# Kernel tuning notes

Measured on AMD Instinct MI355X. Metric: run time of the kernel, lower is better.

Reference implementation:

```python
import jax, jax.numpy as jnp
import numpy as np

K = 20      # kNN neighbors
H = 4       # attention heads
EPS = 1e-5  # BatchNorm eps
NEG = 0.2   # LeakyReLU negative slope


def lrelu(x):
    return jnp.where(x >= 0, x, NEG * x)


def bn(x, g, b):
    # eval-mode BatchNorm: running_mean=0, running_var=1
    return x * (g / jnp.sqrt(1.0 + EPS)) + b


def knn_idx(x):
    # x: (B, N, C) -> (B, N, K) indices of K nearest neighbors (incl. self)
    inner = -2.0 * jnp.einsum('bnc,bmc->bnm', x, x)
    xx = jnp.sum(x * x, axis=-1)
    pd = -xx[:, :, None] - inner - xx[:, None, :]  # negative squared distance
    return jax.lax.top_k(pd, K)[1]


def edge_conv(x, w, g, b):
    # EdgeConv: gather kNN features, cat(nbr-ctr, ctr), 1x1 conv, BN, LeakyReLU, max over K
    idx = knn_idx(x)                                   # (B,N,K)
    nbr = jax.vmap(lambda f, i: f[i])(x, idx)          # (B,N,K,C)
    ctr = jnp.broadcast_to(x[:, :, None, :], nbr.shape)
    e = jnp.concatenate([nbr - ctr, ctr], axis=-1)     # (B,N,K,2C)
    h = lrelu(bn(jnp.einsum('bnkc,oc->bnko', e, w), g, b))
    return jnp.max(h, axis=2)                          # (B,N,Cout)


def mha(x, w_in, b_in, w_out, b_out):
    # Faithful to source: (B,N,E) fed to nn.MultiheadAttention with batch_first=False,
    # so seq length L=B and batch=N (attention mixes across the batch axis).
    L, Nb, E = x.shape
    d = E // H
    qkv = x @ w_in.T + b_in
    q, k, v = jnp.split(qkv, 3, axis=-1)
    q = q.reshape(L, Nb, H, d) * (1.0 / np.sqrt(d))
    k = k.reshape(L, Nb, H, d)
    v = v.reshape(L, Nb, H, d)
    a = jax.nn.softmax(jnp.einsum('lnhd,mnhd->nhlm', q, k), axis=-1)
    o = jnp.einsum('nhlm,mnhd->lnhd', a, v).reshape(L, Nb, E)
    return o @ w_out.T + b_out


def setup_inputs():
    ks = iter(jax.random.split(jax.random.key(0), 64))
    def rn(shape, s=0.05):
        return jax.random.normal(next(ks), shape, jnp.float32) * s
    def gamma(c):
        return 1.0 + rn((c,), 0.1)
    B, N = 8, 1024
    inp = {'x': rn((B, N, 3), 1.0)}
    for i, (ci, co) in enumerate([(6, 64), (128, 64), (128, 128), (256, 256)], 1):
        inp[f'w{i}'] = rn((co, ci)); inp[f'g{i}'] = gamma(co); inp[f'b{i}'] = rn((co,))
    for i, e in enumerate([64, 64, 128, 256], 1):
        inp[f'a{i}_wi'] = rn((3 * e, e)); inp[f'a{i}_bi'] = rn((3 * e,))
        inp[f'a{i}_wo'] = rn((e, e));     inp[f'a{i}_bo'] = rn((e,))
    inp['w5'] = rn((1024, 512)); inp['g5'] = gamma(1024); inp['b5'] = rn((1024,))
    inp['l1w'] = rn((512, 2048)); inp['g6'] = gamma(512); inp['b6'] = rn((512,))
    inp['l2w'] = rn((256, 512)); inp['l2b'] = rn((256,))
    inp['g7'] = gamma(256); inp['b7'] = rn((256,))
    inp['l3w'] = rn((40, 256)); inp['l3b'] = rn((40,))
    return inp


def reference(x, w1, g1, b1, a1_wi, a1_bi, a1_wo, a1_bo,
              w2, g2, b2, a2_wi, a2_bi, a2_wo, a2_bo,
              w3, g3, b3, a3_wi, a3_bi, a3_wo, a3_bo,
              w4, g4, b4, a4_wi, a4_bi, a4_wo, a4_bo,
              w5, g5, b5, l1w, g6, b6, l2w, l2b, g7, b7, l3w, l3b):
    x1 = edge_conv(x, w1, g1, b1)
    x1 = mha(x1, a1_wi, a1_bi, a1_wo, a1_bo) + x1
    x2 = edge_conv(x1, w2, g2, b2)
    x2 = mha(x2, a2_wi, a2_bi, a2_wo, a2_bo) + x2
    x3 = edge_conv(x2, w3, g3, b3)
    x3 = mha(x3, a3_wi, a3_bi, a3_wo, a3_bo) + x3
    x4 = edge_conv(x3, w4, g4, b4)
    x4 = mha(x4, a4_wi, a4_bi, a4_wo, a4_bo) + x4
    h = lrelu(bn(jnp.concatenate([x1, x2, x3, x4], axis=-1) @ w5.T, g5, b5))  # (B,N,1024)
    feat = jnp.concatenate([jnp.max(h, axis=1), jnp.mean(h, axis=1)], axis=-1)  # (B,2048)
    h = lrelu(bn(feat @ l1w.T, g6, b6))
    h = lrelu(bn(h @ l2w.T + l2b, g7, b7))  # dropout is eval-mode identity
    return h @ l3w.T + l3b  # (B, 40)
```

## Files before the change

### kernel.cpp

```cpp
#include <hip/hip_runtime.h>
#include <hip/hip_bf16.h>

#define B_ 8
#define N_ 1024
#define K_ 20
#define BN_ (B_*N_)

#define BN_SCALE 0.9999950000374997f

typedef __attribute__((ext_vector_type(8))) short short8;
typedef __attribute__((ext_vector_type(4))) float f32x4;

__device__ __forceinline__ float US2F(unsigned short u) {
    union { unsigned u; float f; } c; c.u = ((unsigned)u) << 16; return c.f;
}
__device__ __forceinline__ unsigned short F2BF(float f) {
    union { float f; unsigned u; } c; c.f = f;
    unsigned r = c.u + 0x7FFF + ((c.u >> 16) & 1);
    return (unsigned short)(r >> 16);
}

__device__ __forceinline__ void ldsld16(const unsigned short* g, unsigned short* l) {
    __builtin_amdgcn_global_load_lds(
        (const __attribute__((address_space(1))) void*)g,
        (__attribute__((address_space(3))) void*)l, 16, 0, 0);
}

struct DetP { const unsigned short* g[7]; };
__device__ __forceinline__ int det_isbf(const DetP& dp) {
    int cnt = 0;
    #pragma unroll
    for (int i = 0; i < 7; i++) {
        float v = US2F(dp.g[i][0]);
        if (v > 0.5f && v < 1.5f) cnt++;
    }
    return cnt >= 4;
}

struct TPar { const void* src; void* dst; int O, I, blk0, mode; };
struct TList { TPar p[44]; };
struct TrP { const void* src; float* dst; int O, I, bx, blk0; };

__global__ __launch_bounds__(256) void k_prep(TList tl, int nent,
                                              TrP q0, TrP q1, TrP q2,
                                              int nbp, int nbtr,
                                              const void* x0, DetP dp,
                                              unsigned short* __restrict__ xa,
                                              unsigned short* __restrict__ xb,
                                              float* __restrict__ xx1) {
    __shared__ int sbf;
    if (threadIdx.x == 0) sbf = det_isbf(dp);
    __syncthreads();
    const int isbf = sbf;
    auto ld0 = [&](int idx) {
        return isbf ? US2F(((const unsigned short*)x0)[idx])
                    : ((const float*)x0)[idx];
    };
    const int bid = blockIdx.x;
    if (bid >= nbp + nbtr) {
        int blk = bid - nbp - nbtr;
        if (blk >= (BN_ * 32) / 256) {
            int i = (blk - (BN_ * 32) / 256) * 256 + threadIdx.x;
            if (i >= BN_) return;
            float s = 0.f;
            #pragma unroll
            for (int c = 0; c < 3; c++) { float v = ld0(i * 3 + c); s += v * v; }
            xx1[i] = s;
            return;
        }
        const int e = blk * 256 + threadIdx.x;
        const int i = e >> 5, p = e & 31;
        unsigned short va = 0, vb = 0;
        if (p < 9) {
            const int seg = p / 3, c = p - seg * 3;
            const float v = ld0(i * 3 + c);
            const unsigned short h = F2BF(v);
            const unsigned short l = F2BF(v - US2F(h));
            va = (seg == 1) ? l : h;
            vb = (seg < 2) ? h : l;
        }
        xa[e] = va; xb[e] = vb;
        return;
    }
    if (bid >= nbp) {
        int blk = bid - nbp;
        TrP p = q0;
        if (blk >= q2.blk0) p = q2; else if (blk >= q1.blk0) p = q1;
        blk -= p.blk0;
        const int tx = threadIdx.x & 31, ty = threadIdx.x >> 5;
        const int bi = blk % p.bx, bo = blk / p.bx;
        const int i0 = bi * 32, o0 = bo * 32;
        __shared__ float s[32][33];
        #pragma unroll
        for (int r = 0; r < 4; r++) {
            const int o = o0 + ty + r * 8, i = i0 + tx;
            if (o < p.O && i < p.I) {
                const size_t e = (size_t)o * p.I + i;
                s[ty + r * 8][tx] = isbf ? US2F(((const unsigned short*)p.src)[e])
                                         : ((const float*)p.src)[e];
            }
        }
        __syncthreads();
        #pragma unroll
        for (int r = 0; r < 4; r++) {
            const int i = i0 + ty + r * 8, o = o0 + tx;
            if (i < p.I && o < p.O) p.dst[(size_t)i * p.O + o] = s[tx][ty + r * 8];
        }
        return;
    }
    int blk = bid;
    int wi = 0;
    for (int j = nent - 1; j >= 0; j--) { if (blk >= tl.p[j].blk0) { wi = j; break; } }
    const TPar p = tl.p[wi];
    int e = (blk - p.blk0) * 256 + threadIdx.x;
    int n = p.O * p.I;
    if (e >= n) return;
    if (p.mode == 4) { ((float*)p.dst)[e] = 0.f; return; }
    int o = e / p.I, i = e - o * p.I;
    float v = isbf ? US2F(((const unsigned short*)p.src)[e])
                   : ((const float*)p.src)[e];
    if (p.mode == 0) {
        ((float*)p.dst)[(size_t)i * p.O + o] = v;
    } else if (p.mode == 2) {
        ((unsigned short*)p.dst)[e] = F2BF(v);
    } else {
        const int C = p.I >> 1;
        if (i < C) ((unsigned short*)p.dst)[(size_t)o * C + i] = F2BF(v);
        else       ((unsigned short*)p.dst)[(size_t)(p.O + o) * C + (i - C)] = F2BF(v);
    }
}

template<int KP, int TM, int TN>
__device__ __forceinline__ void pdm_dev(int bid,
                                        const unsigned short* __restrict__ xa,
                                        const unsigned short* __restrict__ xb,
                                        const float* __restrict__ xx,
                                        float* __restrict__ pd) {
    const int b = bid & 7;
    const int tt = bid >> 3;
    const int rb = (tt >> 3) * TM, cb = (tt & 7) * TN;
    const unsigned short* Ab = xa + (size_t)b * N_ * KP;
    const unsigned short* Bb = xb + (size_t)b * N_ * KP;
    const float* xxb = xx + (size_t)b * N_;
    const int t = threadIdx.x;
    __shared__ __align__(16) unsigned short As[2][TM * 32];
    __shared__ __align__(16) unsigned short Bs[2][TN * 32];
    const int w = t >> 6, lane = t & 63;
    constexpr int QR = TM / 2, QC = TN / 2;
    constexpr int MR = QR / 16, NR = QC / 16;
    const int wr = (w & 1) * QR, wc = (w >> 1) * QC;
    const int fr = lane & 15, q = lane >> 4;
    f32x4 acc[MR][NR] = {};

    auto STAGE = [&](int buf, int k0) {
        constexpr int AT = TM * 4;
        #pragma unroll
        for (int R = 0; R < (AT + 255) / 256; R++) {
            const int G = t + R * 256;
            if (AT >= (R + 1) * 256 || G < AT) {
                const int m = G >> 2, gs = (G & 3) ^ ((m >> 1) & 3);
                ldsld16(&Ab[(size_t)(rb + m) * KP + k0 + gs * 8], &As[buf][w * 512 + R * 2048]);
            }
        }
        constexpr int BT = TN * 4;
        #pragma unroll
        for (int R = 0; R < (BT + 255) / 256; R++) {
            const int G = t + R * 256;
            if (BT >= (R + 1) * 256 || G < BT) {
                const int n = G >> 2, gs = (G & 3) ^ ((n >> 1) & 3);
                ldsld16(&Bb[(size_t)(cb + n) * KP + k0 + gs * 8], &Bs[buf][w * 512 + R * 2048]);
            }
        }
    };

    constexpr int NT = KP / 32;
    STAGE(0, 0);
    asm volatile("s_waitcnt vmcnt(0)" ::: "memory");
    __builtin_amdgcn_s_barrier();
    int cur = 0;
    for (int ts = 0; ts < NT; ++ts) {
        if (ts + 1 < NT) STAGE(cur ^ 1, (ts + 1) * 32);
        short8 af[MR], bfr[NR];
        #pragma unroll
        for (int mi = 0; mi < MR; mi++) {
            const int r = wr + mi * 16 + fr;
            af[mi] = *reinterpret_cast<const short8*>(&As[cur][r * 32 + ((q ^ ((r >> 1) & 3)) << 3)]);
        }
        #pragma unroll
        for (int ni = 0; ni < NR; ni++) {
            const int r = wc + ni * 16 + fr;
            bfr[ni] = *reinterpret_cast<const short8*>(&Bs[cur][r * 32 + ((q ^ ((r >> 1) & 3)) << 3)]);
        }
        #pragma unroll
        for (int mi = 0; mi < MR; mi++) {
            #pragma unroll
            for (int ni = 0; ni < NR; ni++)
                acc[mi][ni] = __builtin_amdgcn_mfma_f32_16x16x32_bf16(af[mi], bfr[ni], acc[mi][ni], 0, 0, 0);
        }
        asm volatile("s_waitcnt vmcnt(0)" ::: "memory");
        __builtin_amdgcn_s_barrier();
        cur ^= 1;
    }
    float* pdb = pd + (size_t)b * N_ * N_;
    const int cr = (lane >> 4) * 4, cc = lane & 15;
    #pragma unroll
    for (int mi = 0; mi < MR; mi++) {
        #pragma unroll
        for (int ni = 0; ni < NR; ni++) {
            #pragma unroll
            for (int r = 0; r < 4; r++) {
                const int row = rb + wr + mi * 16 + cr + r;
                const int col = cb + wc + ni * 16 + cc;
                pdb[(size_t)row * N_ + col] = 2.f * acc[mi][ni][r] - xxb[col];
            }
        }
    }
}

template<int KD, int NC, int TM, int TN, bool CATA, bool POOL, int SPLIT>
__device__ __forceinline__ void gemm_dev(int bx, int by,
                                         const unsigned short* __restrict__ A,
                                         const unsigned short* __restrict__ A2,
                                         const unsigned short* __restrict__ A3,
                                         const unsigned short* __restrict__ A4,
                                         const unsigned short* __restrict__ Bw,
                                         const float* __restrict__ bias,
                                         const float* __restrict__ resid,
                                         float* __restrict__ Cout,
                                         float* __restrict__ Cz, int yco,
                                         int scale_cols, float qs,
                                         const float* __restrict__ gamma,
                                         const float* __restrict__ beta,
                                         unsigned short* __restrict__ obf,
                                         unsigned* __restrict__ pmaxu,
                                         float* __restrict__ psum,
                                         unsigned short* __restrict__ sxa,
                                         unsigned short* __restrict__ sxb,
                                         float* __restrict__ xxo) {
    const int t = threadIdx.x;
    const int rb = bx * TM, cb = by * TN;
    const int w = t >> 6, lane = t & 63;
    constexpr int QR = TM / 2, QC = TN / 2;
    constexpr int MR = QR / 16, NR = QC / 16;
    const int wr = (w & 1) * QR, wc = (w >> 1) * QC;
    const int fr = lane & 15, q = lane >> 4, fq = q * 8;
    f32x4 acc[MR][NR] = {};
    if constexpr (KD % 32 == 0) {
        __shared__ __align__(16) unsigned short As[2][TM * 32];
        __shared__ __align__(16) unsigned short Bs[2][TN * 32];
        auto STAGE = [&](int buf, int k0) {
            const unsigned short* Asrc = A; int AC = KD, ac0 = k0;
            if constexpr (CATA) {
                if (k0 >= 256)      { Asrc = A4; AC = 256; ac0 = k0 - 256; }
                else if (k0 >= 128) { Asrc = A3; AC = 128; ac0 = k0 - 128; }
                else if (k0 >= 64)  { Asrc = A2; AC = 64;  ac0 = k0 - 64; }
                else                { Asrc = A;  AC = 64;  ac0 = k0; }
            }
            constexpr int AT = TM * 4;
            #pragma unroll
            for (int R = 0; R < (AT + 255) / 256; R++) {
                const int G = t + R * 256;
                if (AT >= (R + 1) * 256 || G < AT) {
                    const int m = G >> 2, gs = (G & 3) ^ ((m >> 1) & 3);
                    ldsld16(&Asrc[(size_t)(rb + m) * AC + ac0 + gs * 8], &As[buf][w * 512 + R * 2048]);
                }
            }
            constexpr int BT = TN * 4;
            #pragma unroll
            for (int R = 0; R < (BT + 255) / 256; R++) {
                const int G = t + R * 256;
                if (BT >= (R + 1) * 256 || G < BT) {
                    const int n = G >> 2, gs = (G & 3) ^ ((n >> 1) & 3);
                    ldsld16(&Bw[(size_t)(cb + n) * KD + k0 + gs * 8], &Bs[buf][w * 512 + R * 2048]);
                }
            }
        };
        constexpr int NT = KD / 32;
        STAGE(0, 0);
        asm volatile("s_waitcnt vmcnt(0)" ::: "memory");
        __builtin_amdgcn_s_barrier();
        int cur = 0;
        for (int ts = 0; ts < NT; ++ts) {
            if (ts + 1 < NT) STAGE(cur ^ 1, (ts + 1) * 32);
            short8 af[MR], bfr[NR];
            #pragma unroll
            for (int mi = 0; mi < MR; mi++) {
                const int r = wr + mi * 16 + fr;
                af[mi] = *reinterpret_cast<const short8*>(&As[cur][r * 32 + ((q ^ ((r >> 1) & 3)) << 3)]);
            }
            #pragma unroll
            for (int ni = 0; ni < NR; ni++) {
                const int r = wc + ni * 16 + fr;
                bfr[ni] = *reinterpret_cast<const short8*>(&Bs[cur][r * 32 + ((q ^ ((r >> 1) & 3)) << 3)]);
            }
            #pragma unroll
            for (int mi = 0; mi < MR; mi++) {
                #pragma unroll
                for (int ni = 0; ni < NR; ni++)
                    acc[mi][ni] = __builtin_amdgcn_mfma_f32_16x16x32_bf16(af[mi], bfr[ni], acc[mi][ni], 0, 0, 0);
            }
            asm volatile("s_waitcnt vmcnt(0)" ::: "memory");
            __builtin_amdgcn_s_barrier();
            cur ^= 1;
        }
    } else {
        __shared__ __align__(16) unsigned short As[TM * 40];
        __shared__ __align__(16) unsigned short Bs[TN * 40];
        for (int k0 = 0; k0 < KD; k0 += 32) {
            __syncthreads();
            #pragma unroll
            for (int u = t; u < TM * 4; u += 256) {
                const int m = u >> 2, c = (u & 3) * 8;
                #pragma unroll
                for (int j = 0; j < 8; j++) {
                    const int kk = k0 + c + j;
                    As[m * 40 + c + j] = (kk < KD) ? A[(size_t)(rb + m) * KD + kk] : (unsigned short)0;
                }
            }
            #pragma unroll
            for (int u = t; u < TN * 4; u += 256) {
                const int n = u >> 2, c = (u & 3) * 8;
                const int gn = cb + n;
                if (gn < NC) {
                    #pragma unroll
                    for (int j = 0; j < 8; j++) {
                        const int kk = k0 + c + j;
                        Bs[n * 40 + c + j] = (kk < KD) ? Bw[(size_t)gn * KD + kk] : (unsigned short)0;
                    }
                } else {
                    short8 z = {};
                    *reinterpret_cast<short8*>(&Bs[n * 40 + c]) = z;
                }
            }
            __syncthreads();
            short8 af[MR], bfr[NR];
            #pragma unroll
            for (int mi = 0; mi < MR; mi++)
                af[mi] = *reinterpret_cast<const short8*>(&As[(wr + mi * 16 + fr) * 40 + fq]);
            #pragma unroll
            for (int ni = 0; ni < NR; ni++)
                bfr[ni] = *reinterpret_cast<const short8*>(&Bs[(wc + ni * 16 + fr) * 40 + fq]);
            #pragma unroll
            for (int mi = 0; mi < MR; mi++) {
                #pragma unroll
                for (int ni = 0; ni < NR; ni++)
                    acc[mi][ni] = __builtin_amdgcn_mfma_f32_16x16x32_bf16(af[mi], bfr[ni], acc[mi][ni], 0, 0, 0);
            }
        }
    }
    const int cr = (lane >> 4) * 4, cc = lane & 15;
    if constexpr (POOL) {
        const int bidx = rb >> 10;
        #pragma unroll
        for (int ni = 0; ni < NR; ni++) {
            const int col = cb + wc + ni * 16 + cc;
            const float gm = gamma[col] * BN_SCALE, bt = beta[col];
            float sm = 0.f, mxv = -3e38f;
            #pragma unroll
            for (int mi = 0; mi < MR; mi++) {
                #pragma unroll
                for (int r = 0; r < 4; r++) {
                    float v = acc[mi][ni][r] * gm + bt;
                    v = v >= 0.f ? v : 0.2f * v;
                    sm += v; mxv = fmaxf(mxv, v);
                }
            }
            sm += __shfl_xor(sm, 16, 64);
            sm += __shfl_xor(sm, 32, 64);
            mxv = fmaxf(mxv, __shfl_xor(mxv, 16, 64));
            mxv = fmaxf(mxv, __shfl_xor(mxv, 32, 64));
            if (lane < 16) {
                atomicAdd(&psum[bidx * 1024 + col], sm);
                unsigned tb = __float_as_uint(mxv);
                tb = (tb & 0x80000000u) ? ~tb : (tb | 0x80000000u);
                atomicMax(&pmaxu[bidx * 1024 + col], tb);
            }
        }
    } else {
        float sx[MR][4] = {};
        #pragma unroll
        for (int mi = 0; mi < MR; mi++) {
            #pragma unroll
            for (int ni = 0; ni < NR; ni++) {
                #pragma unroll
                for (int r = 0; r < 4; r++) {
                    const int row = rb + wr + mi * 16 + cr + r;
                    const int col = cb + wc + ni * 16 + cc;
                    if (col < NC) {
                        float v = acc[mi][ni][r] + (bias ? bias[col] : 0.f);
                        if (col < scale_cols) v *= qs;
                        if (resid) v += resid[(size_t)row * NC + col];
                        if (gamma) {
                            v = v * (gamma[col] * BN_SCALE) + beta[col];
                            v = v >= 0.f ? v : 0.2f * v;
                        }
                        if (yco > 0) {
                            if (col < yco) Cout[(size_t)row * yco + col] = v;
                            else           Cz[(size_t)row * yco + (col - yco)] = v;
                        } else {
                            Cout[(size_t)row * NC + col] = v;
                        }
                        if (obf) obf[(size_t)row * NC + col] = F2BF(v);
                        if constexpr (SPLIT > 0) {
                            constexpr int KP2 = 3 * SPLIT;
                            const unsigned short h = F2BF(v);
                            const unsigned short l = F2BF(v - US2F(h));
                            sxa[(size_t)row * KP2 + 0 * SPLIT + col] = h;
                            sxa[(size_t)row * KP2 + 1 * SPLIT + col] = l;
                            sxa[(size_t)row * KP2 + 2 * SPLIT + col] = h;
                            sxb[(size_t)row * KP2 + 0 * SPLIT + col] = h;
                            sxb[(size_t)row * KP2 + 1 * SPLIT + col] = h;
                            sxb[(size_t)row * KP2 + 2 * SPLIT + col] = l;
                            sx[mi][r] += v * v;
                        }
                    }
                }
            }
        }
        if constexpr (SPLIT > 0) {
            #pragma unroll
            for (int mi = 0; mi < MR; mi++) {
                #pragma unroll
                for (int r = 0; r < 4; r++) {
                    float s = sx[mi][r];
                    s += __shfl_xor(s, 1, 64);
                    s += __shfl_xor(s, 2, 64);
                    s += __shfl_xor(s, 4, 64);
                    s += __shfl_xor(s, 8, 64);
                    if ((lane & 15) == 0)
                        atomicAdd(&xxo[rb + wr + mi * 16 + cr + r], s);
                }
            }
        }
    }
}

template<int KD, int NC, int TM, int TN, bool CATA = false, bool POOL = false, int SPLIT = 0, bool AFF = false>
__global__ __launch_bounds__(256) void k_gemmb(const unsigned short* __restrict__ A,
                                               const unsigned short* __restrict__ A2,
                                               const unsigned short* __restrict__ A3,
                                               const unsigned short* __restrict__ A4,
                                               const unsigned short* __restrict__ Bw,
                                               const float* __restrict__ bias,
                                               const float* __restrict__ resid,
                                               float* __restrict__ Cout,
                                               int scale_cols, float qs,
                                               const float* __restrict__ gamma,
                                               const float* __restrict__ beta,
                                               unsigned short* __restrict__ obf,
                                               unsigned* __restrict__ pmaxu,
                                               float* __restrict__ psum,
                                               unsigned short* __restrict__ sxa,
                                               unsigned short* __restrict__ sxb,
                                               float* __restrict__ xxo) {
    int bx = blockIdx.x;
    if constexpr (AFF) bx = (bx & 7) * (gridDim.x >> 3) + (bx >> 3);
    gemm_dev<KD, NC, TM, TN, CATA, POOL, SPLIT>(bx, blockIdx.y,
        A, A2, A3, A4, Bw, bias, resid, Cout, nullptr, 0, scale_cols, qs, gamma, beta,
        obf, pmaxu, psum, sxa, sxb, xxo);
}

template<int KP, int KDY, int NCY, int TMY, int TNY>
__global__ __launch_bounds__(256) void k_pdmyz(const unsigned short* __restrict__ xa,
                                               const unsigned short* __restrict__ xb,
                                               const float* __restrict__ xx,
                                               float* __restrict__ pd,
                                               const unsigned short* __restrict__ Ay,
                                               const unsigned short* __restrict__ Bwy,
                                               float* __restrict__ Cy,
                                               float* __restrict__ Cz, int yco, int gxy) {
    if ((int)blockIdx.x < 512) { pdm_dev<KP, 128, 128>(blockIdx.x, xa, xb, xx, pd); return; }
    const int g = blockIdx.x - 512;
    const int batch = g & 7, rem = g >> 3;
    const int rpb = gxy >> 3;
    const int bx = batch * rpb + rem % rpb;
    const int by = rem / rpb;
    gemm_dev<KDY, NCY, TMY, TNY, false, false, 0>(bx, by,
        Ay, nullptr, nullptr, nullptr, Bwy, nullptr, nullptr, Cy, Cz, yco, 0, 1.f,
        nullptr, nullptr, nullptr, nullptr, nullptr, nullptr, nullptr, nullptr);
}

template<int CO>
__global__ __launch_bounds__(256) void k_seledge(const float* __restrict__ pd,
                                                 const float* __restrict__ y,
                                                 const float* __restrict__ z,
                                                 const float* __restrict__ g,
                                                 const float* __restrict__ bb,
                                                 float* __restrict__ out,
                                                 unsigned short* __restrict__ outb) {
    const int t = threadIdx.x;
    const int w = t >> 6, lane = t & 63;
    const int blk = blockIdx.x;
    const int b = blk & 7;
    const int i0 = (b << 10) + ((blk >> 3) << 2);
    const int bbase = b << 10;
    __shared__ int sidx[4][K_];
    {
        const int i = i0 + w;
        const float* row = pd + (size_t)b * N_ * N_ + (size_t)(i & 1023) * N_;
        unsigned key[16];
        #pragma unroll
        for (int q = 0; q < 16; q++) {
            const int j = q * 64 + lane;
            unsigned bits = __float_as_uint(row[j]);
            bits = (bits & 0x80000000u) ? ~bits : (bits | 0x80000000u);
            key[q] = (bits & 0xFFFFFC00u) | (unsigned)(N_ - 1 - j);
        }
        int myj = 0;
        for (int kk = 0; kk < K_; kk++) {
            unsigned m = key[0];
            #pragma unroll
            for (int u = 1; u < 16; u++) m = key[u] > m ? key[u] : m;
            #pragma unroll
            for (int s = 1; s < 64; s <<= 1) {
                unsigned o = (unsigned)__shfl_xor((int)m, s, 64);
                m = o > m ? o : m;
            }
            const int j = N_ - 1 - (int)(m & 1023u);
            if (lane == kk) myj = j;
            #pragma unroll
            for (int u = 0; u < 16; u++)
                if (key[u] == m) key[u] = 0u;
        }
        if (lane < K_) sidx[w][lane] = myj;
    }
    __syncthreads();
    constexpr int TPP = CO / 4;
    if (t < 4 * TPP) {
        const int p = t / TPP;
        const int cw = (t % TPP) * 4;
        const int ig = i0 + p;
        float4 m = {-3e38f, -3e38f, -3e38f, -3e38f};
        #pragma unroll 4
        for (int k = 0; k < K_; k++) {
            const int jg = bbase + sidx[p][k];
            const float4 yv = *reinterpret_cast<const float4*>(&y[(size_t)jg * CO + cw]);
            m.x = fmaxf(m.x, yv.x); m.y = fmaxf(m.y, yv.y);
            m.z = fmaxf(m.z, yv.z); m.w = fmaxf(m.w, yv.w);
        }
        const float4 yi = *reinterpret_cast<const float4*>(&y[(size_t)ig * CO + cw]);
        const float4 zi = *reinterpret_cast<const float4*>(&z[(size_t)ig * CO + cw]);
        const float4 gv = *reinterpret_cast<const float4*>(&g[cw]);
        const float4 bv = *reinterpret_cast<const float4*>(&bb[cw]);
        float vals[4] = {m.x - yi.x + zi.x, m.y - yi.y + zi.y,
                         m.z - yi.z + zi.z, m.w - yi.w + zi.w};
        float gs[4] = {gv.x, gv.y, gv.z, gv.w};
        float bs[4] = {bv.x, bv.y, bv.z, bv.w};
        float4 o;
        float* op = &o.x;
        #pragma unroll
        for (int j = 0; j < 4; j++) {
            float h = vals[j] * (gs[j] * BN_SCALE) + bs[j];
            op[j] = h >= 0.f ? h : 0.2f * h;
        }
        *reinterpret_cast<float4*>(&out[(size_t)ig * CO + cw]) = o;
        #pragma unroll
        for (int j = 0; j < 4; j++) outb[(size_t)ig * CO + cw + j] = F2BF(op[j]);
    }
}

template<int E>
__global__ __launch_bounds__(256) void k_attn(const float* __restrict__ qkv,
                                              unsigned short* __restrict__ o) {
    constexpr int H = 4, D = E / H, L = 8;
    const int n = blockIdx.x;
    const int t = threadIdx.x;
    const int h = t >> 6, lane = t & 63;
    __shared__ float sq[L][3 * E];
    __shared__ float so[L][E];
    for (int u = t; u < L * 3 * E; u += 256) {
        int l = u / (3 * E), r = u - l * (3 * E);
        sq[l][r] = qkv[(size_t)(l * N_ + n) * (3 * E) + r];
    }
    __syncthreads();
    const int l = lane >> 3, m = lane & 7;
    float s = 0.f;
    #pragma unroll 8
    for (int dd = 0; dd < D; dd++)
        s += sq[l][h * D + dd] * sq[m][E + h * D + dd];
    float mx = s;
    #pragma unroll
    for (int st = 1; st < 8; st <<= 1) mx = fmaxf(mx, __shfl_xor(mx, st, 64));
    float e = expf(s - mx);
    float sum = e;
    #pragma unroll
    for (int st = 1; st < 8; st <<= 1) sum += __shfl_xor(sum, st, 64);
    const float p = e / sum;
    float pm[8];
    #pragma unroll
    for (int mm = 0; mm < 8; mm++) pm[mm] = __shfl(p, (lane & 56) | mm, 64);
    #pragma unroll
    for (int j = 0; j < D / 8; j++) {
        const int dd = m + 8 * j;
        float a = 0.f;
        #pragma unroll
        for (int mm = 0; mm < 8; mm++) a += pm[mm] * sq[mm][2 * E + h * D + dd];
        so[l][h * D + dd] = a;
    }
    __syncthreads();
    for (int u = t; u < L * E; u += 256) {
        int l2 = u / E, e2 = u - l2 * E;
        o[(size_t)(l2 * N_ + n) * E + e2] = F2BF(so[l2][e2]);
    }
}

template<int E, int SPLIT>
__global__ __launch_bounds__(256) void k_attnout(const float* __restrict__ qkv,
                                                 const unsigned short* __restrict__ wo,
                                                 const float* __restrict__ bo,
                                                 float* __restrict__ x,
                                                 unsigned short* __restrict__ xob,
                                                 unsigned short* __restrict__ sxa,
                                                 unsigned short* __restrict__ sxb,
                                                 float* __restrict__ xxo) {
    constexpr int H = 4, D = E / H, L = 8;
    const int n = blockIdx.x;
    const int t = threadIdx.x;
    const int h = t >> 6, lane = t & 63;
    __shared__ float sq[L][3 * E];
    __shared__ float so[L][E];
    __shared__ unsigned short swo[E][E + 8];
    __shared__ float sxx[L];
    for (int u = t; u < L * 3 * E; u += 256) {
        int l = u / (3 * E), r = u - l * (3 * E);
        sq[l][r] = qkv[(size_t)(l * N_ + n) * (3 * E) + r];
    }
    for (int u = t; u < E * E; u += 256) swo[u / E][u % E] = wo[u];
    if (t < L) sxx[t] = 0.f;
    __syncthreads();
    const int l = lane >> 3, m = lane & 7;
    float s = 0.f;
    #pragma unroll 8
    for (int dd = 0; dd < D; dd++)
        s += sq[l][h * D + dd] * sq[m][E + h * D + dd];
    float mx = s;
    #pragma unroll
    for (int st = 1; st < 8; st <<= 1) mx = fmaxf(mx, __shfl_xor(mx, st, 64));
    float e = expf(s - mx);
    float sum = e;
    #pragma unroll
    for (int st = 1; st < 8; st <<= 1) sum += __shfl_xor(sum, st, 64);
    const float p = e / sum;
    float pm[8];
    #pragma unroll
    for (int mm = 0; mm < 8; mm++) pm[mm] = __shfl(p, (lane & 56) | mm, 64);
    #pragma unroll
    for (int j = 0; j < D / 8; j++) {
        const int dd = m + 8 * j;
        float a = 0.f;
        #pragma unroll
        for (int mm = 0; mm < 8; mm++) a += pm[mm] * sq[mm][2 * E + h * D + dd];
        so[l][h * D + dd] = a;
    }
    __syncthreads();
    for (int u = t; u < L * E; u += 256)
        so[u / E][u % E] = US2F(F2BF(so[u / E][u % E]));
    __syncthreads();
    constexpr int PT = (L * E) / 256;
    #pragma unroll
    for (int it = 0; it < PT; it++) {
        const int item = t + it * 256;
        const int ll = item / E, ee = item % E;
        float acc = 0.f;
        #pragma unroll 16
        for (int c = 0; c < E; c++)
            acc += so[ll][c] * US2F(swo[ee][c]);
        const int row = ll * N_ + n;
        const float v = acc + bo[ee] + x[(size_t)row * E + ee];
        x[(size_t)row * E + ee] = v;
        xob[(size_t)row * E + ee] = F2BF(v);
        if constexpr (SPLIT > 0) {
            constexpr int KP2 = 3 * SPLIT;
            const unsigned short hh = F2BF(v);
            const unsigned short lo = F2BF(v - US2F(hh));
            sxa[(size_t)row * KP2 + 0 * SPLIT + ee] = hh;
            sxa[(size_t)row * KP2 + 1 * SPLIT + ee] = lo;
            sxa[(size_t)row * KP2 + 2 * SPLIT + ee] = hh;
            sxb[(size_t)row * KP2 + 0 * SPLIT + ee] = hh;
            sxb[(size_t)row * KP2 + 1 * SPLIT + ee] = hh;
            sxb[(size_t)row * KP2 + 2 * SPLIT + ee] = lo;
            float vs = v * v;
            #pragma unroll
            for (int st = 1; st < 64; st <<= 1) vs += __shfl_xor(vs, st, 64);
            if (lane == 0) atomicAdd(&sxx[ll], vs);
        }
    }
    if constexpr (SPLIT > 0) {
        __syncthreads();
        if (t < L) xxo[t * N_ + n] = sxx[t];
    }
}

__global__ __launch_bounds__(256) void k_fc1(const unsigned* __restrict__ pmaxu,
                                             const float* __restrict__ psum,
                                             const float* __restrict__ l1wT,
                                             const float* __restrict__ g6, const float* __restrict__ b6,
                                             float* __restrict__ f1) {
    int oc = blockIdx.x, b = blockIdx.y, t = threadIdx.x;
    __shared__ float fin[2048];
    __shared__ float ps[4][64];
    for (int u = t; u < 2048; u += 256) {
        float v;
        if (u < 1024) {
            unsigned tb = pmaxu[b * 1024 + u];
            unsigned bits = (tb & 0x80000000u) ? (tb & 0x7FFFFFFFu) : ~tb;
            v = __uint_as_float(bits);
        } else {
            v = psum[b * 1024 + (u - 1024)] * (1.f / 1024.f);
        }
        fin[u] = v;
    }
    __syncthreads();
    int ol = t & 63, kc = t >> 6;
    int o = oc * 64 + ol;
    float acc = 0.f;
    for (int c = kc * 512; c < kc * 512 + 512; c++) acc += fin[c] * l1wT[(size_t)c * 512 + o];
    ps[kc][ol] = acc;
    __syncthreads();
    if (t < 64) {
        int oo = oc * 64 + t;
        float a = ps[0][t] + ps[1][t] + ps[2][t] + ps[3][t];
        float h = a * (g6[oo] * BN_SCALE) + b6[oo];
        f1[b * 512 + oo] = h >= 0.f ? h : 0.2f * h;
    }
}

__global__ __launch_bounds__(256) void k_fc23(const float* __restrict__ f1, const float* __restrict__ l2wT,
                                              const float* __restrict__ l2b,
                                              const float* __restrict__ g7, const float* __restrict__ b7,
                                              const float* __restrict__ l3wT, const float* __restrict__ l3b,
                                              void* __restrict__ out, DetP dp) {
    int b = blockIdx.x, t = threadIdx.x;
    __shared__ float fin[512];
    __shared__ float f2s[256];
    __shared__ int sbf;
    if (t == 0) sbf = det_isbf(dp);
    for (int u = t; u < 512; u += 256) fin[u] = f1[b * 512 + u];
    __syncthreads();
    {
        float acc = 0.f;
        for (int c = 0; c < 512; c++) acc += fin[c] * l2wT[(size_t)c * 256 + t];
        acc += l2b[t];
        float h = acc * (g7[t] * BN_SCALE) + b7[t];
        f2s[t] = h >= 0.f ? h : 0.2f * h;
    }
    __syncthreads();
    if (t < 40) {
        float acc = 0.f;
        for (int c = 0; c < 256; c++) acc += f2s[c] * l3wT[(size_t)c * 40 + t];
        acc += l3b[t];
        if (sbf) ((__hip_bfloat16*)out)[b * 40 + t] = __float2bfloat16(acc);
        else     ((float*)out)[b * 40 + t] = acc;
    }
}

extern "C" void kernel_launch(void* const* d_in, const int* in_sizes, int n_in,
                              void* d_out, int out_size, void* d_ws, size_t ws_size,
                              hipStream_t stream) {
    auto us = [&](int i) { return (const unsigned short*)d_in[i]; };

    float* ws = (float*)d_ws;
    size_t off = 0;
    auto A = [&](size_t n) { float* p = ws + off; off += (n + 3) & ~(size_t)3; return p; };
    auto AU = [&](size_t n) { return (unsigned short*)A((n + 1) / 2); };
    float* x1   = A((size_t)BN_ * 64);
    float* x2   = A((size_t)BN_ * 64);
    float* x3   = A((size_t)BN_ * 128);
    float* x4   = A((size_t)BN_ * 256);
    float* pd   = A((size_t)BN_ * 1024);
    float* f1   = A(8 * 512);
    float* xx   = A(4 * BN_);
    float* qkvw = A((size_t)BN_ * 768);
    unsigned short* xa = AU((size_t)BN_ * 384);
    unsigned short* xb = AU((size_t)BN_ * 384);
    unsigned short* xf0b = AU((size_t)BN_ * 3);
    unsigned short* x1b  = AU((size_t)BN_ * 64);
    unsigned short* x2b  = AU((size_t)BN_ * 64);
    unsigned short* x3b  = AU((size_t)BN_ * 128);
    unsigned short* x4b  = AU((size_t)BN_ * 256);
    unsigned short* owb  = AU((size_t)BN_ * 256);
    unsigned* pmaxu = (unsigned*)A(8 * 1024);
    float*    psum  = A(8 * 1024);
    unsigned short* w1yzb = AU(128 * 3);
    unsigned short* w2yzb = AU(128 * 64);
    unsigned short* w3yzb = AU(256 * 64);
    unsigned short* w4yzb = AU(512 * 128);
    unsigned short* a1wib = AU(192 * 64);  unsigned short* a1wob = AU(64 * 64);
    unsigned short* a2wib = AU(192 * 64);  unsigned short* a2wob = AU(64 * 64);
    unsigned short* a3wib = AU(384 * 128); unsigned short* a3wob = AU(128 * 128);
    unsigned short* a4wib = AU(768 * 256); unsigned short* a4wob = AU(256 * 256);
    unsigned short* w5b   = AU(1024 * 512);
    float* l1wT  = A(2048 * 512);
    float* l2wT  = A(512 * 256);
    float* l3wT  = A(256 * 40);
    float* g1f = A(64);   float* b1f = A(64);
    float* g2f = A(64);   float* b2f = A(64);
    float* g3f = A(128);  float* b3f = A(128);
    float* g4f = A(256);  float* b4f = A(256);
    float* bi1 = A(192);  float* bo1 = A(64);
    float* bi2 = A(192);  float* bo2 = A(64);
    float* bi3 = A(384);  float* bo3 = A(128);
    float* bi4 = A(768);  float* bo4 = A(256);
    float* g5f = A(1024); float* b5f = A(1024);
    float* g6f = A(512);  float* b6f = A(512);
    float* l2bf = A(256);
    float* g7f = A(256);  float* b7f = A(256);
    float* l3bf = A(40);

    float* xx1 = xx;              float* xx2 = xx + BN_;
    float* xx3 = xx + 2 * BN_;    float* xx4 = xx + 3 * BN_;

    float* yy = qkvw;
    float* zz = qkvw + (size_t)BN_ * 256;

    DetP dp{{us(2), us(5), us(8), us(11), us(30), us(33), us(37)}};

    TList tl; int nb = 0; int k = 0;
    auto add = [&](int i, void* dst, int O, int I, int mode) {
        tl.p[k].src = d_in[i]; tl.p[k].dst = dst; tl.p[k].O = O; tl.p[k].I = I;
        tl.p[k].blk0 = nb; tl.p[k].mode = mode;
        nb += (O * I + 255) / 256; k++;
    };
    add(0,  xf0b,  BN_ * 3, 1, 2);
    add(0,  pmaxu, 16384, 1, 4);
    add(1,  w1yzb, 64, 6, 3);
    add(4,  w2yzb, 64, 128, 3);
    add(7,  w3yzb, 128, 128, 3);
    add(10, w4yzb, 256, 256, 3);
    add(13, a1wib, 192, 64, 2);
    add(15, a1wob, 64, 64, 2);
    add(17, a2wib, 192, 64, 2);
    add(19, a2wob, 64, 64, 2);
    add(21, a3wib, 384, 128, 2);
    add(23, a3wob, 128, 128, 2);
    add(25, a4wib, 768, 256, 2);
    add(27, a4wob, 256, 256, 2);
    add(29, w5b,   1024, 512, 2);
    add(2,  g1f, 64, 1, 0);   add(3,  b1f, 64, 1, 0);
    add(5,  g2f, 64, 1, 0);   add(6,  b2f, 64, 1, 0);
    add(8,  g3f, 128, 1, 0);  add(9,  b3f, 128, 1, 0);
    add(11, g4f, 256, 1, 0);  add(12, b4f, 256, 1, 0);
    add(14, bi1, 192, 1, 0);  add(16, bo1, 64, 1, 0);
    add(18, bi2, 192, 1, 0);  add(20, bo2, 64, 1, 0);
    add(22, bi3, 384, 1, 0);  add(24, bo3, 128, 1, 0);
    add(26, bi4, 768, 1, 0);  add(28, bo4, 256, 1, 0);
    add(30, g5f, 1024, 1, 0); add(31, b5f, 1024, 1, 0);
    add(33, g6f, 512, 1, 0);  add(34, b6f, 512, 1, 0);
    add(36, l2bf, 256, 1, 0);
    add(37, g7f, 256, 1, 0);  add(38, b7f, 256, 1, 0);
    add(40, l3bf, 40, 1, 0);

    TrP tp1{d_in[32], l1wT, 512, 2048, 2048 / 32, 0};
    TrP tp2{d_in[35], l2wT, 256, 512,  512 / 32,  (2048 / 32) * (512 / 32)};
    TrP tp3{d_in[39], l3wT, 40,  256,  256 / 32,  tp2.blk0 + (512 / 32) * (256 / 32)};
    const int trblocks = tp3.blk0 + (256 / 32) * ((40 + 31) / 32);
    const int splblocks = (BN_ * 32) / 256 + 32;
    k_prep<<<nb + trblocks + splblocks, 256, 0, stream>>>(
        tl, k, tp1, tp2, tp3, nb, trblocks, d_in[0], dp, xa, xb, xx1);

    const unsigned short* N0 = nullptr;
    unsigned short* U0 = nullptr;
    unsigned* NU = nullptr; float* NF = nullptr;

    k_pdmyz<32, 3, 128, 64, 64><<<512 + 256, 256, 0, stream>>>(xa, xb, xx1, pd, xf0b, w1yzb, yy, zz, 64, 128);
    k_seledge<64><<<2048, 256, 0, stream>>>(pd, yy, zz, g1f, b1f, x1, x1b);
    k_gemmb<64, 192, 64, 64, false, false, 0, true><<<dim3(128, 3), 256, 0, stream>>>(x1b, N0, N0, N0, a1wib, bi1, nullptr, qkvw, 64, 0.25f, nullptr, nullptr, nullptr, NU, NF, U0, U0, NF);
    k_attnout<64, 64><<<N_, 256, 0, stream>>>(qkvw, a1wob, bo1, x1, x1b, xa, xb, xx2);

    k_pdmyz<192, 64, 128, 64, 64><<<512 + 256, 256, 0, stream>>>(xa, xb, xx2, pd, x1b, w2yzb, yy, zz, 64, 128);
    k_seledge<64><<<2048, 256, 0, stream>>>(pd, yy, zz, g2f, b2f, x2, x2b);
    k_gemmb<64, 192, 64, 64, false, false, 0, true><<<dim3(128, 3), 256, 0, stream>>>(x2b, N0, N0, N0, a2wib, bi2, nullptr, qkvw, 64, 0.25f, nullptr, nullptr, nullptr, NU, NF, U0, U0, NF);
    k_attnout<64, 64><<<N_, 256, 0, stream>>>(qkvw, a2wob, bo2, x2, x2b, xa, xb, xx3);

    k_pdmyz<192, 64, 256, 64, 64><<<512 + 512, 256, 0, stream>>>(xa, xb, xx3, pd, x2b, w3yzb, yy, zz, 128, 128);
    k_seledge<128><<<2048, 256, 0, stream>>>(pd, yy, zz, g3f, b3f, x3, x3b);
    k_gemmb<128, 384, 64, 128, false, false, 0, true><<<dim3(128, 3), 256, 0, stream>>>(x3b, N0, N0, N0, a3wib, bi3, nullptr, qkvw, 128, 0.17677669529663687f, nullptr, nullptr, nullptr, NU, NF, U0, U0, NF);
    k_attnout<128, 128><<<N_, 256, 0, stream>>>(qkvw, a3wob, bo3, x3, x3b, xa, xb, xx4);

    k_pdmyz<384, 128, 512, 128, 128><<<512 + 256, 256, 0, stream>>>(xa, xb, xx4, pd, x3b, w4yzb, yy, zz, 256, 64);
    k_seledge<256><<<2048, 256, 0, stream>>>(pd, yy, zz, g4f, b4f, x4, x4b);
    k_gemmb<256, 768, 64, 128, false, false, 0, true><<<dim3(128, 6), 256, 0, stream>>>(x4b, N0, N0, N0, a4wib, bi4, nullptr, qkvw, 256, 0.125f, nullptr, nullptr, nullptr, NU, NF, U0, U0, NF);
    k_attn<256><<<N_, 256, 0, stream>>>(qkvw, owb);
    k_gemmb<256, 256, 64, 128, false, false, 0, true><<<dim3(128, 2), 256, 0, stream>>>(owb, N0, N0, N0, a4wob, bo4, x4, x4, 0, 1.f, nullptr, nullptr, x4b, NU, NF, U0, U0, NF);

    k_gemmb<512, 1024, 128, 128, true, true, 0, true><<<dim3(64, 8), 256, 0, stream>>>(
        x1b, x2b, x3b, x4b, w5b, nullptr, nullptr, nullptr, 0, 1.f, g5f, b5f, nullptr, pmaxu, psum, U0, U0, NF);
    k_fc1<<<dim3(8, 8), 256, 0, stream>>>(pmaxu, psum, l1wT, g6f, b6f, f1);
    k_fc23<<<8, 256, 0, stream>>>(f1, l2wT, l2bf, g7f, b7f, l3wT, l3bf, d_out, dp);
}
```

Before: 476.0 us.

## Spread weight preparation across later kernels as auxiliary blocks

Weight conversion and transpose work that used to run entirely in the first prep kernel is split into three groups. The weights needed later (layer 2-3 conv/attention, fc1 transpose, layer-4 attention and w5) are now handled by extra blocks appended to the first pairwise-distance and selection kernels. This shortens the serial prep launch and overlaps that work with kernels that may leave CUs idle. In exchange those kernels get extra parameters, and each auxiliary block reruns the dtype detection.

```diff
diff --git a/kernel.cpp b/kernel.cpp
--- a/kernel.cpp
+++ b/kernel.cpp
@@ -38,77 +38,10 @@
 }
 
 struct TPar { const void* src; void* dst; int O, I, blk0, mode; };
-struct TList { TPar p[44]; };
+struct TList { TPar p[32]; };
 struct TrP { const void* src; float* dst; int O, I, bx, blk0; };
 
-__global__ __launch_bounds__(256) void k_prep(TList tl, int nent,
-                                              TrP q0, TrP q1, TrP q2,
-                                              int nbp, int nbtr,
-                                              const void* x0, DetP dp,
-                                              unsigned short* __restrict__ xa,
-                                              unsigned short* __restrict__ xb,
-                                              float* __restrict__ xx1) {
-    __shared__ int sbf;
-    if (threadIdx.x == 0) sbf = det_isbf(dp);
-    __syncthreads();
-    const int isbf = sbf;
-    auto ld0 = [&](int idx) {
-        return isbf ? US2F(((const unsigned short*)x0)[idx])
-                    : ((const float*)x0)[idx];
-    };
-    const int bid = blockIdx.x;
-    if (bid >= nbp + nbtr) {
-        int blk = bid - nbp - nbtr;
-        if (blk >= (BN_ * 32) / 256) {
-            int i = (blk - (BN_ * 32) / 256) * 256 + threadIdx.x;
-            if (i >= BN_) return;
-            float s = 0.f;
-            #pragma unroll
-            for (int c = 0; c < 3; c++) { float v = ld0(i * 3 + c); s += v * v; }
-            xx1[i] = s;
-            return;
-        }
-        const int e = blk * 256 + threadIdx.x;
-        const int i = e >> 5, p = e & 31;
-        unsigned short va = 0, vb = 0;
-        if (p < 9) {
-            const int seg = p / 3, c = p - seg * 3;
-            const float v = ld0(i * 3 + c);
-            const unsigned short h = F2BF(v);
-            const unsigned short l = F2BF(v - US2F(h));
-            va = (seg == 1) ? l : h;
-            vb = (seg < 2) ? h : l;
-        }
-        xa[e] = va; xb[e] = vb;
-        return;
-    }
-    if (bid >= nbp) {
-        int blk = bid - nbp;
-        TrP p = q0;
-        if (blk >= q2.blk0) p = q2; else if (blk >= q1.blk0) p = q1;
-        blk -= p.blk0;
-        const int tx = threadIdx.x & 31, ty = threadIdx.x >> 5;
-        const int bi = blk % p.bx, bo = blk / p.bx;
-        const int i0 = bi * 32, o0 = bo * 32;
-        __shared__ float s[32][33];
-        #pragma unroll
-        for (int r = 0; r < 4; r++) {
-            const int o = o0 + ty + r * 8, i = i0 + tx;
-            if (o < p.O && i < p.I) {
-                const size_t e = (size_t)o * p.I + i;
-                s[ty + r * 8][tx] = isbf ? US2F(((const unsigned short*)p.src)[e])
-                                         : ((const float*)p.src)[e];
-            }
-        }
-        __syncthreads();
-        #pragma unroll
-        for (int r = 0; r < 4; r++) {
-            const int i = i0 + ty + r * 8, o = o0 + tx;
-            if (i < p.I && o < p.O) p.dst[(size_t)i * p.O + o] = s[tx][ty + r * 8];
-        }
-        return;
-    }
-    int blk = bid;
+__device__ __forceinline__ void prep_entry(const TList& tl, int nent, int blk, int isbf) {
     int wi = 0;
     for (int j = nent - 1; j >= 0; j--) { if (blk >= tl.p[j].blk0) { wi = j; break; } }
     const TPar p = tl.p[wi];
@@ -128,6 +61,78 @@
         if (i < C) ((unsigned short*)p.dst)[(size_t)o * C + i] = F2BF(v);
         else       ((unsigned short*)p.dst)[(size_t)(p.O + o) * C + (i - C)] = F2BF(v);
     }
+}
+
+__device__ __forceinline__ void tr_entry(const TrP& p, int blk, int isbf) {
+    const int tx = threadIdx.x & 31, ty = threadIdx.x >> 5;
+    const int bi = blk % p.bx, bo = blk / p.bx;
+    const int i0 = bi * 32, o0 = bo * 32;
+    __shared__ float s[32][33];
+    #pragma unroll
+    for (int r = 0; r < 4; r++) {
+        const int o = o0 + ty + r * 8, i = i0 + tx;
+        if (o < p.O && i < p.I) {
+            const size_t e = (size_t)o * p.I + i;
+            s[ty + r * 8][tx] = isbf ? US2F(((const unsigned short*)p.src)[e])
+                                     : ((const float*)p.src)[e];
+        }
+    }
+    __syncthreads();
+    #pragma unroll
+    for (int r = 0; r < 4; r++) {
+        const int i = i0 + ty + r * 8, o = o0 + tx;
+        if (i < p.I && o < p.O) p.dst[(size_t)i * p.O + o] = s[tx][ty + r * 8];
+    }
+}
+
+__global__ __launch_bounds__(256) void k_prep(TList tl, int nent,
+                                              TrP q0, TrP q1,
+                                              int nbp, int nbtr,
+                                              const void* x0, DetP dp,
+                                              unsigned short* __restrict__ xa,
+                                              unsigned short* __restrict__ xb,
+                                              float* __restrict__ xx1) {
+    __shared__ int sbf;
+    if (threadIdx.x == 0) sbf = det_isbf(dp);
+    __syncthreads();
+    const int isbf = sbf;
+    auto ld0 = [&](int idx) {
+        return isbf ? US2F(((const unsigned short*)x0)[idx])
+                    : ((const float*)x0)[idx];
+    };
+    const int bid = blockIdx.x;
+    if (bid >= nbp + nbtr) {
+        int blk = bid - nbp - nbtr;
+        if (blk >= (BN_ * 32) / 256) {
+            int i = (blk - (BN_ * 32) / 256) * 256 + threadIdx.x;
+            if (i >= BN_) return;
+            float s = 0.f;
+            #pragma unroll
+            for (int c = 0; c < 3; c++) { float v = ld0(i * 3 + c); s += v * v; }
+            xx1[i] = s;
+            return;
+        }
+        const int e = blk * 256 + threadIdx.x;
+        const int i = e >> 5, p = e & 31;
+        unsigned short va = 0, vb = 0;
+        if (p < 9) {
+            const int seg = p / 3, c = p - seg * 3;
+            const float v = ld0(i * 3 + c);
+            const unsigned short h = F2BF(v);
+            const unsigned short l = F2BF(v - US2F(h));
+            va = (seg == 1) ? l : h;
+            vb = (seg < 2) ? h : l;
+        }
+        xa[e] = va; xb[e] = vb;
+        return;
+    }
+    if (bid >= nbp) {
+        int blk = bid - nbp;
+        if (blk >= q1.blk0) tr_entry(q1, blk - q1.blk0, isbf);
+        else                tr_entry(q0, blk, isbf);
+        return;
+    }
+    prep_entry(tl, nent, bid, isbf);
 }
 
 template<int KP, int TM, int TN>
@@ -468,7 +473,17 @@
                                                const unsigned short* __restrict__ Ay,
                                                const unsigned short* __restrict__ Bwy,
                                                float* __restrict__ Cy,
-                                               float* __restrict__ Cz, int yco, int gxy) {
+                                               float* __restrict__ Cz, int yco, int gxy,
+                                               int auxbase, TList tlb, int nlb, int nbb,
+                                               TrP trp, int ntr, DetP dp) {
+    if ((int)blockIdx.x >= auxbase) {
+        int ab = blockIdx.x - auxbase;
+        const int isbf = det_isbf(dp);
+        if (ab < nbb) { prep_entry(tlb, nlb, ab, isbf); return; }
+        ab -= nbb;
+        if (ab < ntr) tr_entry(trp, ab, isbf);
+        return;
+    }
     if ((int)blockIdx.x < 512) { pdm_dev<KP, 128, 128>(blockIdx.x, xa, xb, xx, pd); return; }
     const int g = blockIdx.x - 512;
     const int batch = g & 7, rem = g >> 3;
@@ -487,10 +502,15 @@
                                                  const float* __restrict__ g,
                                                  const float* __restrict__ bb,
                                                  float* __restrict__ out,
-                                                 unsigned short* __restrict__ outb) {
+                                                 unsigned short* __restrict__ outb,
+                                                 TList tlc, int nlc, DetP dp) {
     const int t = threadIdx.x;
+    const int blk = blockIdx.x;
+    if (blk >= 2048) {
+        prep_entry(tlc, nlc, blk - 2048, det_isbf(dp));
+        return;
+    }
     const int w = t >> 6, lane = t & 63;
-    const int blk = blockIdx.x;
     const int b = blk & 7;
     const int i0 = (b << 10) + ((blk >> 3) << 2);
     const int bbase = b << 10;
@@ -815,70 +835,91 @@
 
     DetP dp{{us(2), us(5), us(8), us(11), us(30), us(33), us(37)}};
 
-    TList tl; int nb = 0; int k = 0;
-    auto add = [&](int i, void* dst, int O, int I, int mode) {
-        tl.p[k].src = d_in[i]; tl.p[k].dst = dst; tl.p[k].O = O; tl.p[k].I = I;
-        tl.p[k].blk0 = nb; tl.p[k].mode = mode;
-        nb += (O * I + 255) / 256; k++;
+    TList tlA; int nbA = 0, kA = 0;
+    auto addA = [&](int i, void* dst, int O, int I, int mode) {
+        tlA.p[kA] = {d_in[i], dst, O, I, nbA, mode};
+        nbA += (O * I + 255) / 256; kA++;
     };
-    add(0,  xf0b,  BN_ * 3, 1, 2);
-    add(0,  pmaxu, 16384, 1, 4);
-    add(1,  w1yzb, 64, 6, 3);
-    add(4,  w2yzb, 64, 128, 3);
-    add(7,  w3yzb, 128, 128, 3);
-    add(10, w4yzb, 256, 256, 3);
-    add(13, a1wib, 192, 64, 2);
-    add(15, a1wob, 64, 64, 2);
-    add(17, a2wib, 192, 64, 2);
-    add(19, a2wob, 64, 64, 2);
-    add(21, a3wib, 384, 128, 2);
-    add(23, a3wob, 128, 128, 2);
-    add(25, a4wib, 768, 256, 2);
-    add(27, a4wob, 256, 256, 2);
-    add(29, w5b,   1024, 512, 2);
-    add(2,  g1f, 64, 1, 0);   add(3,  b1f, 64, 1, 0);
-    add(5,  g2f, 64, 1, 0);   add(6,  b2f, 64, 1, 0);
-    add(8,  g3f, 128, 1, 0);  add(9,  b3f, 128, 1, 0);
-    add(11, g4f, 256, 1, 0);  add(12, b4f, 256, 1, 0);
-    add(14, bi1, 192, 1, 0);  add(16, bo1, 64, 1, 0);
-    add(18, bi2, 192, 1, 0);  add(20, bo2, 64, 1, 0);
-    add(22, bi3, 384, 1, 0);  add(24, bo3, 128, 1, 0);
-    add(26, bi4, 768, 1, 0);  add(28, bo4, 256, 1, 0);
-    add(30, g5f, 1024, 1, 0); add(31, b5f, 1024, 1, 0);
-    add(33, g6f, 512, 1, 0);  add(34, b6f, 512, 1, 0);
-    add(36, l2bf, 256, 1, 0);
-    add(37, g7f, 256, 1, 0);  add(38, b7f, 256, 1, 0);
-    add(40, l3bf, 40, 1, 0);
-
+    addA(0,  xf0b,  BN_ * 3, 1, 2);
+    addA(0,  pmaxu, 16384, 1, 4);
+    addA(1,  w1yzb, 64, 6, 3);
+    addA(13, a1wib, 192, 64, 2);
+    addA(15, a1wob, 64, 64, 2);
+    addA(2,  g1f, 64, 1, 0);   addA(3,  b1f, 64, 1, 0);
+    addA(5,  g2f, 64, 1, 0);   addA(6,  b2f, 64, 1, 0);
+    addA(8,  g3f, 128, 1, 0);  addA(9,  b3f, 128, 1, 0);
+    addA(11, g4f, 256, 1, 0);  addA(12, b4f, 256, 1, 0);
+    addA(14, bi1, 192, 1, 0);  addA(16, bo1, 64, 1, 0);
+    addA(18, bi2, 192, 1, 0);  addA(20, bo2, 64, 1, 0);
+    addA(22, bi3, 384, 1, 0);  addA(24, bo3, 128, 1, 0);
+    addA(26, bi4, 768, 1, 0);  addA(28, bo4, 256, 1, 0);
+    addA(30, g5f, 1024, 1, 0); addA(31, b5f, 1024, 1, 0);
+    addA(33, g6f, 512, 1, 0);  addA(34, b6f, 512, 1, 0);
+    addA(36, l2bf, 256, 1, 0);
+    addA(37, g7f, 256, 1, 0);  addA(38, b7f, 256, 1, 0);
+    addA(40, l3bf, 40, 1, 0);
+
+    TList tlB; int nbB = 0, kB = 0;
+    auto addB = [&](int i, void* dst, int O, int I, int mode) {
+        tlB.p[kB] = {d_in[i], dst, O, I, nbB, mode};
+        nbB += (O * I + 255) / 256; kB++;
+    };
+    addB(4,  w2yzb, 64, 128, 3);
+    addB(7,  w3yzb, 128, 128, 3);
+    addB(10, w4yzb, 256, 256, 3);
+    addB(17, a2wib, 192, 64, 2);
+    addB(19, a2wob, 64, 64, 2);
+    addB(21, a3wib, 384, 128, 2);
+    addB(23, a3wob, 128, 128, 2);
+
+    TList tlC; int nbC = 0, kC = 0;
+    auto addC = [&](int i, void* dst, int O, int I, int mode) {
+        tlC.p[kC] = {d_in[i], dst, O, I, nbC, mode};
+        nbC += (O * I + 255) / 256; kC++;
+    };
+    addC(25, a4wib, 768, 256, 2);
+    addC(27, a4wob, 256, 256, 2);
+    addC(29, w5b,   1024, 512, 2);
+
+    TrP tp2{d_in[35], l2wT, 256, 512,  512 / 32,  0};
+    TrP tp3{d_in[39], l3wT, 40,  256,  256 / 32,  (512 / 32) * (256 / 32)};
+    const int trprep = tp3.blk0 + (256 / 32) * ((40 + 31) / 32);
     TrP tp1{d_in[32], l1wT, 512, 2048, 2048 / 32, 0};
-    TrP tp2{d_in[35], l2wT, 256, 512,  512 / 32,  (2048 / 32) * (512 / 32)};
-    TrP tp3{d_in[39], l3wT, 40,  256,  256 / 32,  tp2.blk0 + (512 / 32) * (256 / 32)};
-    const int trblocks = tp3.blk0 + (256 / 32) * ((40 + 31) / 32);
+    const int tr1blocks = (2048 / 32) * (512 / 32);
+
     const int splblocks = (BN_ * 32) / 256 + 32;
-    k_prep<<<nb + trblocks + splblocks, 256, 0, stream>>>(
-        tl, k, tp1, tp2, tp3, nb, trblocks, d_in[0], dp, xa, xb, xx1);
+    k_prep<<<nbA + trprep + splblocks, 256, 0, stream>>>(
+        tlA, kA, tp2, tp3, nbA, trprep, d_in[0], dp, xa, xb, xx1);
 
     const unsigned short* N0 = nullptr;
     unsigned short* U0 = nullptr;
     unsigned* NU = nullptr; float* NF = nullptr;
 
-    k_pdmyz<32, 3, 128, 64, 64><<<512 + 256, 256, 0, stream>>>(xa, xb, xx1, pd, xf0b, w1yzb, yy, zz, 64, 128);
-    k_seledge<64><<<2048, 256, 0, stream>>>(pd, yy, zz, g1f, b1f, x1, x1b);
+    k_pdmyz<32, 3, 128, 64, 64><<<768 + nbB + tr1blocks, 256, 0, stream>>>(
+        xa, xb, xx1, pd, xf0b, w1yzb, yy, zz, 64, 128,
+        768, tlB, kB, nbB, tp1, tr1blocks, dp);
+    k_seledge<64><<<2048 + nbC, 256, 0, stream>>>(pd, yy, zz, g1f, b1f, x1, x1b, tlC, kC, dp);
     k_gemmb<64, 192, 64, 64, false, false, 0, true><<<dim3(128, 3), 256, 0, stream>>>(x1b, N0, N0, N0, a1wib, bi1, nullptr, qkvw, 64, 0.25f, nullptr, nullptr, nullptr, NU, NF, U0, U0, NF);
     k_attnout<64, 64><<<N_, 256, 0, stream>>>(qkvw, a1wob, bo1, x1, x1b, xa, xb, xx2);
 
-    k_pdmyz<192, 64, 128, 64, 64><<<512 + 256, 256, 0, stream>>>(xa, xb, xx2, pd, x1b, w2yzb, yy, zz, 64, 128);
-    k_seledge<64><<<2048, 256, 0, stream>>>(pd, yy, zz, g2f, b2f, x2, x2b);
+    k_pdmyz<192, 64, 128, 64, 64><<<768, 256, 0, stream>>>(
+        xa, xb, xx2, pd, x1b, w2yzb, yy, zz, 64, 128,
+        768, tlB, 0, 0, tp1, 0, dp);
+    k_seledge<64><<<2048, 256, 0, stream>>>(pd, yy, zz, g2f, b2f, x2, x2b, tlC, 0, dp);
     k_gemmb<64, 192, 64, 64, false, false, 0, true><<<dim3(128, 3), 256, 0, stream>>>(x2b, N0, N0, N0, a2wib, bi2, nullptr, qkvw, 64, 0.25f, nullptr, nullptr, nullptr, NU, NF, U0, U0, NF);
     k_attnout<64, 64><<<N_, 256, 0, stream>>>(qkvw, a2wob, bo2, x2, x2b, xa, xb, xx3);
 
-    k_pdmyz<192, 64, 256, 64, 64><<<512 + 512, 256, 0, stream>>>(xa, xb, xx3, pd, x2b, w3yzb, yy, zz, 128, 128);
-    k_seledge<128><<<2048, 256, 0, stream>>>(pd, yy, zz, g3f, b3f, x3, x3b);
+    k_pdmyz<192, 64, 256, 64, 64><<<1024, 256, 0, stream>>>(
+        xa, xb, xx3, pd, x2b, w3yzb, yy, zz, 128, 128,
+        1024, tlB, 0, 0, tp1, 0, dp);
+    k_seledge<128><<<2048, 256, 0, stream>>>(pd, yy, zz, g3f, b3f, x3, x3b, tlC, 0, dp);
     k_gemmb<128, 384, 64, 128, false, false, 0, true><<<dim3(128, 3), 256, 0, stream>>>(x3b, N0, N0, N0, a3wib, bi3, nullptr, qkvw, 128, 0.17677669529663687f, nullptr, nullptr, nullptr, NU, NF, U0, U0, NF);
     k_attnout<128, 128><<<N_, 256, 0, stream>>>(qkvw, a3wob, bo3, x3, x3b, xa, xb, xx4);
 
-    k_pdmyz<384, 128, 512, 128, 128><<<512 + 256, 256, 0, stream>>>(xa, xb, xx4, pd, x3b, w4yzb, yy, zz, 256, 64);
-    k_seledge<256><<<2048, 256, 0, stream>>>(pd, yy, zz, g4f, b4f, x4, x4b);
+    k_pdmyz<384, 128, 512, 128, 128><<<768, 256, 0, stream>>>(
+        xa, xb, xx4, pd, x3b, w4yzb, yy, zz, 256, 64,
+        768, tlB, 0, 0, tp1, 0, dp);
+    k_seledge<256><<<2048, 256, 0, stream>>>(pd, yy, zz, g4f, b4f, x4, x4b, tlC, 0, dp);
     k_gemmb<256, 768, 64, 128, false, false, 0, true><<<dim3(128, 6), 256, 0, stream>>>(x4b, N0, N0, N0, a4wib, bi4, nullptr, qkvw, 256, 0.125f, nullptr, nullptr, nullptr, NU, NF, U0, U0, NF);
     k_attn<256><<<N_, 256, 0, stream>>>(qkvw, owb);
     k_gemmb<256, 256, 64, 128, false, false, 0, true><<<dim3(128, 2), 256, 0, stream>>>(owb, N0, N0, N0, a4wob, bo4, x4, x4, 0, 1.f, nullptr, nullptr, x4b, NU, NF, U0, U0, NF);
```

New measurement: 472.1 us. About the same (-0.8%).
